# Kernel tuning notes

Hardware: AMD Instinct MI355X
Metric: run time of the kernel (lower is better)

The kernel has to match this reference:

```python
import jax, jax.numpy as jnp
import numpy as np

B, S, D, E = 2, 2048, 1024, 8
H = 2 * D          # hidden_dim = 2*n_embd
A = H // 16        # adapt_dim


def _ln(x, g, b):
    m = x.mean(-1, keepdims=True)
    v = x.var(-1, keepdims=True)
    return (x - m) * jax.lax.rsqrt(v + 1e-5) * g + b


def setup_inputs() -> dict:
    key = jax.random.key(0)
    ks = jax.random.split(key, 16)
    s = 1.0 / np.sqrt(D)        # shared-linear init scale
    sa = s * 0.01               # adapter-linear init scale
    sg = 0.01 / np.sqrt(A)      # expert adapter init scale
    f32 = jnp.float32
    return {
        "x": jax.random.normal(ks[0], (B, S, D), f32),
        "expert_weights": jax.nn.softmax(jax.random.normal(ks[1], (B * S, E), f32), -1),
        "up_w": jax.random.normal(ks[2], (H, D), f32) * s,
        "gate_w": jax.random.normal(ks[3], (H, D), f32) * s,
        "down_w": jax.random.normal(ks[4], (D, H), f32) * s,
        "pre_w": jax.random.normal(ks[5], (A, D), f32) * sa,
        "post_w": jax.random.normal(ks[6], (A, H), f32) * sa,
        "an_g": jnp.ones((A,), f32),
        "an_b": jnp.zeros((A,), f32),
        "adapt_proj_w": jax.random.normal(ks[7], (H, A), f32) * sa,
        "adapter_w": jax.random.normal(ks[8], (E, A, A), f32) * sg,
        "adapter_g": jnp.ones((E, A), f32),
        "adapter_b": jnp.zeros((E, A), f32),
        "expert_proj_w": jax.random.normal(ks[9], (H, A), f32) * sg,
        "output_proj_w": jax.random.normal(ks[10], (D, H), f32) * sg,
    }


def reference(x, expert_weights, up_w, gate_w, down_w, pre_w, post_w, an_g, an_b,
              adapt_proj_w, adapter_w, adapter_g, adapter_b, expert_proj_w, output_proj_w):
    # ---- SharedExpertMLP ----
    up = x @ up_w.T                                  # [B,S,H]
    gate = x @ gate_w.T                              # [B,S,H]
    hidden = jax.nn.silu(gate) * up                  # SwiGLU
    adapt_in = _ln(x @ pre_w.T, an_g, an_b)          # [B,S,A]
    adapt_out = _ln(hidden @ post_w.T, an_g, an_b)   # [B,S,A]
    w = jnp.einsum('bsa,bta->bst', adapt_in, adapt_out)
    w = jax.nn.silu(jnp.clip(w, -5.0, 5.0))          # clamp+SiLU score
    # explicit fp32 bmm as in original autocast-disabled block
    adapt = jnp.einsum('bst,bta->bsa',
                       w.astype(jnp.float32),
                       adapt_in.astype(jnp.float32)).astype(x.dtype)
    hidden = hidden + 0.1 * (adapt @ adapt_proj_w.T)
    shared_out = hidden @ down_w.T                   # [B,S,D] (dropout is identity in eval)

    # ---- per-token expert mixing ----
    xf = x.reshape(-1, x.shape[-1])                  # [N,D], N=B*S
    a = _ln(xf @ pre_w.T, an_g, an_b)                # [N,A]
    h = jnp.einsum('na,eca->nec', a, adapter_w)      # per-expert low-rank adapt [N,E,A]
    h = _ln(h, adapter_g[None], adapter_b[None])
    mixed = jnp.einsum('ne,nea->na', expert_weights, h)   # combine experts [N,A]
    out = (mixed @ expert_proj_w.T) @ output_proj_w.T     # [N,D]
    return shared_out + out.reshape(x.shape)
```

## Files before the change

kernel.cpp:

```cpp
#include <hip/hip_runtime.h>
#include <hip/hip_bf16.h>
#include <math.h>

#define Bq 2
#define Sq 2048
#define Dq 1024
#define Eq 8
#define Hq 2048
#define Aq 128
#define Nq (Bq*Sq)

typedef __attribute__((ext_vector_type(4))) float f32x4;
typedef __attribute__((ext_vector_type(8))) short bfrag;

__device__ __forceinline__ float silu_f(float x) {
    return x / (1.0f + expf(-x));
}
__device__ __forceinline__ unsigned short f2bf(float x) {
    unsigned u = __float_as_uint(x);
    u += 0x7fffu + ((u >> 16) & 1u);
    return (unsigned short)(u >> 16);
}
__device__ __forceinline__ float bf2f(unsigned short h) {
    return __uint_as_float(((unsigned)h) << 16);
}
__device__ __forceinline__ void gl16(const unsigned short* g, unsigned short* l) {
    __builtin_amdgcn_global_load_lds(
        (const __attribute__((address_space(1))) void*)g,
        (__attribute__((address_space(3))) void*)(void*)l, 16, 0, 0);
}

#define WAITV_BAR(N)                                            \
    asm volatile("s_waitcnt vmcnt(" #N ")" ::: "memory");       \
    __builtin_amdgcn_s_barrier();                               \
    asm volatile("" ::: "memory")
#define END_BAR()                                               \
    asm volatile("" ::: "memory");                              \
    __builtin_amdgcn_s_barrier();                               \
    asm volatile("" ::: "memory")

__global__ __launch_bounds__(256)
void convert_all(const float* __restrict__ x,  const float* __restrict__ gw,
                 const float* __restrict__ uw, const float* __restrict__ dw,
                 const float* __restrict__ pw, const float* __restrict__ ow,
                 const float* __restrict__ opw, const float* __restrict__ aw,
                 unsigned short* xh,  unsigned short* gwh, unsigned short* uwh,
                 unsigned short* dwh, unsigned short* pwh, unsigned short* powh,
                 unsigned short* oph, unsigned short* adw)
{
    const int T = 3276800;
    for (int i = blockIdx.x * 256 + threadIdx.x; i < T; i += gridDim.x * 256) {
        const float* in; unsigned short* hi; int j = i;
        if (j < 1048576)                 { in = x;   hi = xh;  }
        else if ((j -= 1048576) < 524288){ in = gw;  hi = gwh; }
        else if ((j -= 524288) < 524288) { in = uw;  hi = uwh; }
        else if ((j -= 524288) < 524288) { in = dw;  hi = dwh; }
        else if ((j -= 524288) < 32768)  { in = pw;  hi = pwh; }
        else if ((j -= 32768) < 65536)   { in = ow;  hi = powh; }
        else if ((j -= 65536) < 524288)  { in = opw; hi = oph; }
        else { j -= 524288;                in = aw;  hi = adw; }
        float4 v = ((const float4*)in)[j];
        ((ushort4*)hi)[j] = make_ushort4(f2bf(v.x), f2bf(v.y), f2bf(v.z), f2bf(v.w));
    }
}

template<typename TIN>
__global__ __launch_bounds__(256)
void transb(const TIN* __restrict__ in0, const TIN* __restrict__ in1,
            unsigned short* __restrict__ out, int R, int C)
{
    __shared__ float t[32][33];
    const TIN* in = blockIdx.z ? in1 : in0;
    if (!in1) in = in0 + (size_t)blockIdx.z * R * C;
    out += (size_t)blockIdx.z * R * C;
    int tx = threadIdx.x & 31, ty = threadIdx.x >> 5;
    int r0 = blockIdx.y * 32, c0 = blockIdx.x * 32;
#pragma unroll
    for (int j = 0; j < 4; j++) {
        TIN v = in[(size_t)(r0 + ty + j * 8) * C + c0 + tx];
        float f;
        if (sizeof(TIN) == 2) f = bf2f(*(const unsigned short*)&v);
        else                  f = *(const float*)&v;
        t[ty + j * 8][tx] = f;
    }
    __syncthreads();
#pragma unroll
    for (int j = 0; j < 4; j++)
        out[(size_t)(c0 + ty + j * 8) * R + r0 + tx] = f2bf(t[tx][ty + j * 8]);
}

template<int EPI>
__global__ __launch_bounds__(512)
void mg(const unsigned short* __restrict__ Ah, const unsigned short* __restrict__ Bh,
        void* __restrict__ Cv, int N, int K, int kchunks,
        long zA, long zB, long zC, long pz)
{
    __shared__ __align__(16) unsigned short lds[32768];

    const int tid = threadIdx.x;
    const int l   = tid & 63;
    const int w   = tid >> 6;
    const int wr  = w >> 2, wc = w & 3;
    const int bm0 = blockIdx.y * 128, bn0 = blockIdx.x * 128;
    const int bz  = blockIdx.z / kchunks;
    const int kz  = blockIdx.z - bz * kchunks;
    const int kcnt = K / kchunks;
    const int kbeg = kz * kcnt;
    const int kend = kbeg + kcnt;

    const unsigned short* A0 = Ah + (size_t)bz * zA;
    const unsigned short* B0 = Bh + (size_t)bz * zB;

    const int srow = tid >> 3;
    const int sq   = (tid & 7) ^ (srow & 7);
    const size_t aoff = (size_t)(bm0 + srow) * K + sq * 8;
    const size_t boff = (size_t)(bn0 + srow) * K + sq * 8;
    const size_t r64  = (size_t)64 * K;

    auto stage = [&](int b, int kt) {
        unsigned short* d = &lds[b * 16384 + (w << 9)];
        gl16(A0 + aoff + kt,       d + 0);
        gl16(A0 + aoff + kt + r64, d + 4096);
        gl16(B0 + boff + kt,       d + 8192);
        gl16(B0 + boff + kt + r64, d + 12288);
    };

    const int rowa = (wr * 64 + (l & 15)) * 64;
    const int rowb = (wc * 32 + (l & 15)) * 64;
    const int q0 = (((l >> 4)    ) ^ (l & 7)) << 3;
    const int q1 = (((l >> 4) + 4) ^ (l & 7)) << 3;

    f32x4 acc[4][2];
#pragma unroll
    for (int i = 0; i < 4; i++)
#pragma unroll
        for (int j = 0; j < 2; j++) acc[i][j] = (f32x4){0.f, 0.f, 0.f, 0.f};

    stage(0, kbeg);
    int cur = 0;
    for (int kt = kbeg; kt < kend; kt += 64) {
        if (kt + 64 < kend) {
            stage(cur ^ 1, kt + 64);
            WAITV_BAR(4);
        } else {
            WAITV_BAR(0);
        }
        const int cb = cur * 16384;
#pragma unroll
        for (int ks = 0; ks < 2; ks++) {
            const int qo = ks ? q1 : q0;
            bfrag a4[4], b4[2];
#pragma unroll
            for (int f = 0; f < 4; f++)
                a4[f] = *(const bfrag*)&lds[cb + rowa + f * 1024 + qo];
#pragma unroll
            for (int f = 0; f < 2; f++)
                b4[f] = *(const bfrag*)&lds[cb + 8192 + rowb + f * 1024 + qo];
#pragma unroll
            for (int i = 0; i < 4; i++)
#pragma unroll
                for (int j = 0; j < 2; j++)
                    acc[i][j] = __builtin_amdgcn_mfma_f32_16x16x32_bf16(a4[i], b4[j], acc[i][j], 0, 0, 0);
        }
        END_BAR();
        cur ^= 1;
    }

    const int crow0 = bm0 + wr * 64 + (l >> 4) * 4;
    const int ccol0 = bn0 + wc * 32 + (l & 15);
#pragma unroll
    for (int i = 0; i < 4; i++)
#pragma unroll
        for (int j = 0; j < 2; j++)
#pragma unroll
            for (int r = 0; r < 4; r++) {
                size_t idx = (size_t)(crow0 + i * 16 + r) * N + (ccol0 + j * 16);
                float v = acc[i][j][r];
                if (EPI == 0)
                    ((float*)Cv + (size_t)bz * zC + (size_t)kz * pz)[idx] = v;
                else
                    ((unsigned short*)Cv + (size_t)bz * zC)[idx] =
                        f2bf(silu_f(fminf(fmaxf(v, -5.f), 5.f)));
            }
}

__global__ __launch_bounds__(512)
void gsc(const unsigned short* __restrict__ ainh, const unsigned short* __restrict__ aouth,
         const unsigned short* __restrict__ ainT, float* __restrict__ p3)
{
    __shared__ __align__(16) unsigned short lds[65536];
    const int AIN = 0, AOUT = 16384, AINT = 32768, PB = 49152;

    const int tid = threadIdx.x;
    const int l   = tid & 63;
    const int w   = tid >> 6;
    const int wr  = w >> 2, wc = w & 3;
    const int tz  = blockIdx.x;
    const int ib  = blockIdx.y;
    const int b   = blockIdx.z;
    const long SA = (long)Sq * Aq;

    auto stage32 = [&](int base, const unsigned short* src, size_t kstride) {
#pragma unroll
        for (int rd = 0; rd < 4; rd++) {
            int grow = rd * 32 + (w << 2) + (l >> 4);
            int slot = (l & 15) ^ (grow & 15);
            gl16(src + (size_t)grow * kstride + slot * 8,
                 &lds[base + rd * 4096 + (w << 9)]);
        }
    };

    const unsigned short* ainI_src = ainh + (size_t)b * SA + (size_t)(ib * 128) * Aq;
    f32x4 acc2[4][2];
#pragma unroll
    for (int i = 0; i < 4; i++)
#pragma unroll
        for (int j = 0; j < 2; j++) acc2[i][j] = (f32x4){0.f, 0.f, 0.f, 0.f};

    {
        int tglob = tz * 2;
        stage32(AIN,  ainI_src, Aq);
        stage32(AOUT, aouth + (size_t)b * SA + (size_t)(tglob * 128) * Aq, Aq);
        stage32(AINT, ainT  + (size_t)b * SA + (size_t)(tglob * 128), Sq);
        WAITV_BAR(0);
    }

    const int rowa = (wr * 64 + (l & 15)) * 128;
    const int rowb = (wc * 32 + (l & 15)) * 128;

#pragma unroll 1
    for (int t = 0; t < 2; t++) {
        if (t == 1) {
            int tglob = tz * 2 + 1;
            stage32(AOUT, aouth + (size_t)b * SA + (size_t)(tglob * 128) * Aq, Aq);
            stage32(AINT, ainT  + (size_t)b * SA + (size_t)(tglob * 128), Sq);
            WAITV_BAR(0);
        }
        f32x4 acc1[4][2];
#pragma unroll
        for (int i = 0; i < 4; i++)
#pragma unroll
            for (int j = 0; j < 2; j++) acc1[i][j] = (f32x4){0.f, 0.f, 0.f, 0.f};
#pragma unroll
        for (int ks = 0; ks < 4; ks++) {
            const int qo = ((ks * 4 + (l >> 4)) ^ (l & 15)) << 3;
            bfrag a4[4], b4[2];
#pragma unroll
            for (int f = 0; f < 4; f++)
                a4[f] = *(const bfrag*)&lds[AIN + rowa + f * 2048 + qo];
#pragma unroll
            for (int f = 0; f < 2; f++)
                b4[f] = *(const bfrag*)&lds[AOUT + rowb + f * 2048 + qo];
#pragma unroll
            for (int i = 0; i < 4; i++)
#pragma unroll
                for (int j = 0; j < 2; j++)
                    acc1[i][j] = __builtin_amdgcn_mfma_f32_16x16x32_bf16(a4[i], b4[j], acc1[i][j], 0, 0, 0);
        }
        {
            const int prow0 = wr * 64 + (l >> 4) * 4;
            const int pcol0 = wc * 32 + (l & 15);
#pragma unroll
            for (int i = 0; i < 4; i++)
#pragma unroll
                for (int j = 0; j < 2; j++)
#pragma unroll
                    for (int r = 0; r < 4; r++) {
                        int pr = prow0 + i * 16 + r;
                        int pc = pcol0 + j * 16;
                        float v = silu_f(fminf(fmaxf(acc1[i][j][r], -5.f), 5.f));
                        lds[PB + pr * 128 + (((pc >> 3) ^ (pr & 15)) << 3) + (pc & 7)] = f2bf(v);
                    }
        }
        __syncthreads();
#pragma unroll
        for (int ks = 0; ks < 4; ks++) {
            const int qo = ((ks * 4 + (l >> 4)) ^ (l & 15)) << 3;
            bfrag a4[4], b4[2];
#pragma unroll
            for (int f = 0; f < 4; f++)
                a4[f] = *(const bfrag*)&lds[PB + rowa + f * 2048 + qo];
#pragma unroll
            for (int f = 0; f < 2; f++)
                b4[f] = *(const bfrag*)&lds[AINT + rowb + f * 2048 + qo];
#pragma unroll
            for (int i = 0; i < 4; i++)
#pragma unroll
                for (int j = 0; j < 2; j++)
                    acc2[i][j] = __builtin_amdgcn_mfma_f32_16x16x32_bf16(a4[i], b4[j], acc2[i][j], 0, 0, 0);
        }
        __syncthreads();
    }

    const int crow0 = wr * 64 + (l >> 4) * 4;
    const int ccol0 = wc * 32 + (l & 15);
    float* dst = p3 + ((size_t)(b * 8 + tz) * Sq + ib * 128) * Aq;
#pragma unroll
    for (int i = 0; i < 4; i++)
#pragma unroll
        for (int j = 0; j < 2; j++)
#pragma unroll
            for (int r = 0; r < 4; r++)
                dst[(size_t)(crow0 + i * 16 + r) * Aq + ccol0 + j * 16] = acc2[i][j][r];
}

__global__ __launch_bounds__(512)
void gup(const unsigned short* __restrict__ xh, const unsigned short* __restrict__ gwh,
         const unsigned short* __restrict__ uwh, unsigned short* __restrict__ hh)
{
    __shared__ __align__(16) unsigned short lds[24576];
    const int tid = threadIdx.x;
    const int l   = tid & 63;
    const int w   = tid >> 6;
    const int wr  = w >> 2, wc = w & 3;

    int id  = blockIdx.y * gridDim.x + blockIdx.x;
    int xcd = id & 7, j = id >> 3;
    int bx  = (xcd & 1) * 8 + (j & 7);
    int by  = (xcd >> 1) * 8 + (j >> 3);
    const int bm0 = by * 128, bn0 = bx * 128;

    const int srow = tid >> 2;
    const int sq   = (tid & 3) ^ ((srow >> 1) & 3);
    const size_t aoff = (size_t)(bm0 + srow) * Dq + sq * 8;
    const size_t boff = (size_t)(bn0 + srow) * Dq + sq * 8;

    const int rowa = (wr * 64 + (l & 15)) * 32;
    const int rowb = (wc * 32 + (l & 15)) * 32;
    const int q0 = (((l >> 4)) ^ (((l & 15) >> 1) & 3)) << 3;

    auto stage = [&](int b, int kt) {
        unsigned short* d = &lds[b * 12288 + (w << 9)];
        gl16(xh  + aoff + kt, d + 0);
        gl16(gwh + boff + kt, d + 4096);
        gl16(uwh + boff + kt, d + 8192);
    };

    f32x4 accg[4][2], accu[4][2];
#pragma unroll
    for (int i = 0; i < 4; i++)
#pragma unroll
        for (int jj = 0; jj < 2; jj++) {
            accg[i][jj] = (f32x4){0.f, 0.f, 0.f, 0.f};
            accu[i][jj] = (f32x4){0.f, 0.f, 0.f, 0.f};
        }

    stage(0, 0);
    int cur = 0;
    for (int kt = 0; kt < Dq; kt += 32) {
        if (kt + 32 < Dq) {
            stage(cur ^ 1, kt + 32);
            WAITV_BAR(3);
        } else {
            WAITV_BAR(0);
        }
        const int cb = cur * 12288;
        bfrag a4[4], g4[2], u4[2];
#pragma unroll
        for (int f = 0; f < 4; f++)
            a4[f] = *(const bfrag*)&lds[cb + rowa + f * 512 + q0];
#pragma unroll
        for (int f = 0; f < 2; f++) {
            g4[f] = *(const bfrag*)&lds[cb + 4096 + rowb + f * 512 + q0];
            u4[f] = *(const bfrag*)&lds[cb + 8192 + rowb + f * 512 + q0];
        }
#pragma unroll
        for (int i = 0; i < 4; i++)
#pragma unroll
            for (int jj = 0; jj < 2; jj++) {
                accg[i][jj] = __builtin_amdgcn_mfma_f32_16x16x32_bf16(a4[i], g4[jj], accg[i][jj], 0, 0, 0);
                accu[i][jj] = __builtin_amdgcn_mfma_f32_16x16x32_bf16(a4[i], u4[jj], accu[i][jj], 0, 0, 0);
            }
        END_BAR();
        cur ^= 1;
    }

    const int crow0 = bm0 + wr * 64 + (l >> 4) * 4;
    const int ccol0 = bn0 + wc * 32 + (l & 15);
#pragma unroll
    for (int i = 0; i < 4; i++)
#pragma unroll
        for (int jj = 0; jj < 2; jj++)
#pragma unroll
            for (int r = 0; r < 4; r++) {
                size_t idx = (size_t)(crow0 + i * 16 + r) * Hq + (ccol0 + jj * 16);
                hh[idx] = f2bf(silu_f(accg[i][jj][r]) * accu[i][jj][r]);
            }
}

__global__ __launch_bounds__(512)
void gfinal(const unsigned short* __restrict__ hh, const unsigned short* __restrict__ dwh,
            const unsigned short* __restrict__ acat, const unsigned short* __restrict__ kcat,
            float* __restrict__ out)
{
    __shared__ __align__(16) unsigned short lds[49152];
    const int tid = threadIdx.x;
    const int l   = tid & 63;
    const int w   = tid >> 6;
    const int wr  = w >> 2, wc = w & 3;

    int nb  = gridDim.x * gridDim.y;
    int id  = blockIdx.y * gridDim.x + blockIdx.x;
    int id2 = (id & 7) * (nb >> 3) + (id >> 3);
    int bx  = id2 % gridDim.x, by = id2 / gridDim.x;
    const int bm0 = by * 128, bn0 = bx * 128;

    const int srow = tid >> 3;
    const int sq   = (tid & 7) ^ (srow & 7);
    const int rowa = (wr * 64 + (l & 15)) * 64;
    const int rowb = (wc * 32 + (l & 15)) * 64;
    const int q0 = (((l >> 4)    ) ^ (l & 7)) << 3;
    const int q1 = (((l >> 4) + 4) ^ (l & 7)) << 3;

    f32x4 acc[4][2];
#pragma unroll
    for (int i = 0; i < 4; i++)
#pragma unroll
        for (int j = 0; j < 2; j++) acc[i][j] = (f32x4){0.f, 0.f, 0.f, 0.f};

    {
        const size_t aoff = (size_t)(bm0 + srow) * Hq + sq * 8;
        const size_t boff = (size_t)(bn0 + srow) * Hq + sq * 8;
        const size_t r64  = (size_t)64 * Hq;
        auto stage = [&](int b, int kt) {
            unsigned short* d = &lds[b * 16384 + (w << 9)];
            gl16(hh  + aoff + kt,       d + 0);
            gl16(hh  + aoff + kt + r64, d + 4096);
            gl16(dwh + boff + kt,       d + 8192);
            gl16(dwh + boff + kt + r64, d + 12288);
        };
        stage(0, 0);
        stage(1, 64);
        int cur = 0;
        for (int kt = 0; kt < Hq; kt += 64) {
            if (kt + 64 < Hq) { WAITV_BAR(4); } else { WAITV_BAR(0); }
            if (kt + 128 < Hq) {
                int nb3 = (cur + 2 >= 3) ? cur - 1 : cur + 2;
                stage(nb3, kt + 128);
            }
            const int cb = cur * 16384;
#pragma unroll
            for (int ks = 0; ks < 2; ks++) {
                const int qo = ks ? q1 : q0;
                bfrag a4[4], b4[2];
#pragma unroll
                for (int f = 0; f < 4; f++)
                    a4[f] = *(const bfrag*)&lds[cb + rowa + f * 1024 + qo];
#pragma unroll
                for (int f = 0; f < 2; f++)
                    b4[f] = *(const bfrag*)&lds[cb + 8192 + rowb + f * 1024 + qo];
#pragma unroll
                for (int i = 0; i < 4; i++)
#pragma unroll
                    for (int j = 0; j < 2; j++)
                        acc[i][j] = __builtin_amdgcn_mfma_f32_16x16x32_bf16(a4[i], b4[j], acc[i][j], 0, 0, 0);
            }
            cur = (cur == 2) ? 0 : cur + 1;
        }
    }
    END_BAR();
    {
        const size_t aoff = (size_t)(bm0 + srow) * 256 + sq * 8;
        const size_t boff = (size_t)(bn0 + srow) * 256 + sq * 8;
        const size_t r64  = (size_t)64 * 256;
        auto stage2 = [&](int b, int kt) {
            unsigned short* d = &lds[b * 16384 + (w << 9)];
            gl16(acat + aoff + kt,       d + 0);
            gl16(acat + aoff + kt + r64, d + 4096);
            gl16(kcat + boff + kt,       d + 8192);
            gl16(kcat + boff + kt + r64, d + 12288);
        };
        stage2(0, 0);
        stage2(1, 64);
        int cur = 0;
        for (int kt = 0; kt < 256; kt += 64) {
            if (kt + 64 < 256) { WAITV_BAR(4); } else { WAITV_BAR(0); }
            if (kt + 128 < 256) {
                int nb3 = (cur + 2 >= 3) ? cur - 1 : cur + 2;
                stage2(nb3, kt + 128);
            }
            const int cb = cur * 16384;
#pragma unroll
            for (int ks = 0; ks < 2; ks++) {
                const int qo = ks ? q1 : q0;
                bfrag a4[4], b4[2];
#pragma unroll
                for (int f = 0; f < 4; f++)
                    a4[f] = *(const bfrag*)&lds[cb + rowa + f * 1024 + qo];
#pragma unroll
                for (int f = 0; f < 2; f++)
                    b4[f] = *(const bfrag*)&lds[cb + 8192 + rowb + f * 1024 + qo];
#pragma unroll
                for (int i = 0; i < 4; i++)
#pragma unroll
                    for (int j = 0; j < 2; j++)
                        acc[i][j] = __builtin_amdgcn_mfma_f32_16x16x32_bf16(a4[i], b4[j], acc[i][j], 0, 0, 0);
            }
            cur = (cur == 2) ? 0 : cur + 1;
        }
    }

    const int crow0 = bm0 + wr * 64 + (l >> 4) * 4;
    const int ccol0 = bn0 + wc * 32 + (l & 15);
#pragma unroll
    for (int i = 0; i < 4; i++)
#pragma unroll
        for (int j = 0; j < 2; j++)
#pragma unroll
            for (int r = 0; r < 4; r++)
                out[(size_t)(crow0 + i * 16 + r) * Dq + ccol0 + j * 16] = acc[i][j][r];
}

template<int NZ>
__global__ __launch_bounds__(256)
void rln(const float* __restrict__ p, unsigned short* __restrict__ oh,
         const float* __restrict__ g, const float* __restrict__ b, long pstride)
{
    int row  = blockIdx.x * 4 + (threadIdx.x >> 6);
    int lane = threadIdx.x & 63;
    long base = (long)row * Aq;
    float x0 = 0.f, x1 = 0.f;
#pragma unroll
    for (int z = 0; z < NZ; z++) {
        x0 += p[base + z * pstride + lane];
        x1 += p[base + z * pstride + lane + 64];
    }
    float s  = x0 + x1;
    float ss = x0 * x0 + x1 * x1;
#pragma unroll
    for (int off = 32; off > 0; off >>= 1) {
        s  += __shfl_xor(s, off);
        ss += __shfl_xor(ss, off);
    }
    float m  = s * (1.0f / Aq);
    float v  = ss * (1.0f / Aq) - m * m;
    float rs = rsqrtf(v + 1e-5f);
    oh[base + lane]      = f2bf((x0 - m) * rs * g[lane]      + b[lane]);
    oh[base + lane + 64] = f2bf((x1 - m) * rs * g[lane + 64] + b[lane + 64]);
}

template<int NZ>
__global__ __launch_bounds__(256)
void rbf(const float* __restrict__ p, unsigned short* __restrict__ o,
         int rowsPerB, float scale, int total, int ostride, int ocol, int ocolStep)
{
    int i = blockIdx.x * 256 + threadIdx.x;
    if (i >= total) return;
    int n = i >> 7, a = i & 127;
    int bz = n / rowsPerB, s = n - bz * rowsPerB;
    long base = ((long)bz * NZ) * rowsPerB * Aq + (long)s * Aq + a;
    float acc = 0.f;
#pragma unroll
    for (int z = 0; z < NZ; z++) acc += p[base + (long)z * rowsPerB * Aq];
    o[(long)s * ostride + (ocol + bz * ocolStep) + a +
      (ocolStep ? 0 : (long)bz * rowsPerB * ostride)] = f2bf(acc * scale);
}

__global__ __launch_bounds__(256)
void mix_ln(const float* __restrict__ h, const float* __restrict__ ew,
            const float* __restrict__ g, const float* __restrict__ bb,
            unsigned short* __restrict__ acat)
{
    int n    = blockIdx.x * 4 + (threadIdx.x >> 6);
    int lane = threadIdx.x & 63;
    float a0 = 0.0f, a1 = 0.0f;
#pragma unroll
    for (int e = 0; e < Eq; e++) {
        const float* r = h + ((long)e * Nq + n) * Aq;
        float x0 = r[lane], x1 = r[lane + 64];
        float s  = x0 + x1;
        float ss = x0 * x0 + x1 * x1;
#pragma unroll
        for (int off = 32; off > 0; off >>= 1) {
            s  += __shfl_xor(s, off);
            ss += __shfl_xor(ss, off);
        }
        float m  = s * (1.0f / Aq);
        float v  = ss * (1.0f / Aq) - m * m;
        float rs = rsqrtf(v + 1e-5f);
        float wv = ew[(long)n * Eq + e];
        a0 += wv * ((x0 - m) * rs * g[e * Aq + lane]      + bb[e * Aq + lane]);
        a1 += wv * ((x1 - m) * rs * g[e * Aq + lane + 64] + bb[e * Aq + lane + 64]);
    }
    acat[(long)n * 256 + 128 + lane]      = f2bf(a0);
    acat[(long)n * 256 + 128 + lane + 64] = f2bf(a1);
}

extern "C" void kernel_launch(void* const* d_in, const int* in_sizes, int n_in,
                              void* d_out, int out_size, void* d_ws, size_t ws_size,
                              hipStream_t stream)
{
    const float* x             = (const float*)d_in[0];
    const float* ew            = (const float*)d_in[1];
    const float* up_w          = (const float*)d_in[2];
    const float* gate_w        = (const float*)d_in[3];
    const float* down_w        = (const float*)d_in[4];
    const float* pre_w         = (const float*)d_in[5];
    const float* post_w        = (const float*)d_in[6];
    const float* an_g          = (const float*)d_in[7];
    const float* an_b          = (const float*)d_in[8];
    const float* adapt_proj_w  = (const float*)d_in[9];
    const float* adapter_w     = (const float*)d_in[10];
    const float* adapter_g     = (const float*)d_in[11];
    const float* adapter_b     = (const float*)d_in[12];
    const float* expert_proj_w = (const float*)d_in[13];
    const float* output_proj_w = (const float*)d_in[14];
    float* out = (float*)d_out;

#define OFF(kb) ((char*)d_ws + (size_t)(kb) * 1024)
    float* kdp  = (float*)OFF(0);
    float* wfp  = (float*)OFF(8192);
    float* p1   = (float*)OFF(16384);
    float* p2   = (float*)OFF(0);
    float* p3   = (float*)OFF(0);
    float* h_e  = (float*)OFF(0);
    unsigned short* hh   = (unsigned short*)OFF(32768);
    unsigned short* xh   = (unsigned short*)OFF(49152);
    unsigned short* gwh  = (unsigned short*)OFF(57344);
    unsigned short* uwh  = (unsigned short*)OFF(61440);
    unsigned short* dwh  = (unsigned short*)OFF(65536);
    unsigned short* oph  = (unsigned short*)OFF(69632);
    unsigned short* pwh  = (unsigned short*)OFF(73728);
    unsigned short* powh = (unsigned short*)OFF(73984);
    unsigned short* apT  = (unsigned short*)OFF(74496);
    unsigned short* epT  = (unsigned short*)OFF(75008);
    unsigned short* ainh = (unsigned short*)OFF(75520);
    unsigned short* ainT = (unsigned short*)OFF(76544);
    unsigned short* aouth= (unsigned short*)OFF(77568);
    unsigned short* adw  = (unsigned short*)OFF(78592);
    unsigned short* kcat = (unsigned short*)OFF(78848);
    unsigned short* acat = (unsigned short*)OFF(79360);
#undef OFF

    dim3 blk(256), blk512(512);
    const long NA = (long)Nq * Aq;
    const long SA = (long)Sq * Aq;
    const long SS = (long)Sq * Sq;

    convert_all<<<dim3(2048), blk, 0, stream>>>(x, gate_w, up_w, down_w, pre_w, post_w,
        output_proj_w, adapter_w, xh, gwh, uwh, dwh, pwh, powh, oph, adw);
    transb<float><<<dim3(4, 64, 2), blk, 0, stream>>>(adapt_proj_w, expert_proj_w,
        apT, Hq, Aq);

    mg<0><<<dim3(1, 8, 32), blk512, 0, stream>>>(dwh, apT, kdp, Aq, Hq, 16,
        (long)Dq * Hq, (long)Aq * Hq, (long)16 * Dq * Aq, (long)Dq * Aq);
    rbf<16><<<dim3(1024), blk, 0, stream>>>(kdp, kcat, Dq, 1.0f, 2 * Dq * Aq, 256, 0, 128);

    mg<0><<<dim3(1, 32, 8), blk512, 0, stream>>>(xh, pwh, p1, Aq, Dq, 8, 0, 0, 0, NA);
    rln<8><<<dim3(1024), blk, 0, stream>>>(p1, ainh, an_g, an_b, NA);
    transb<unsigned short><<<dim3(4, 64, 2), blk, 0, stream>>>(ainh, nullptr,
        ainT, Sq, Aq);

    gup<<<dim3(16, 32), blk512, 0, stream>>>(xh, gwh, uwh, hh);

    mg<0><<<dim3(1, 32, 8), blk512, 0, stream>>>(hh, powh, p2, Aq, Hq, 8, 0, 0, 0, NA);
    rln<8><<<dim3(1024), blk, 0, stream>>>(p2, aouth, an_g, an_b, NA);

    gsc<<<dim3(8, 16, 2), blk512, 0, stream>>>(ainh, aouth, ainT, p3);
    rbf<8><<<dim3(2048), blk, 0, stream>>>(p3, acat, Sq, 0.1f, Nq * Aq, 256, 0, 0);

    mg<0><<<dim3(1, 32, 8), blk512, 0, stream>>>(ainh, adw, h_e, Aq, Aq, 1,
        0, (long)Aq * Aq, NA, 0);
    mix_ln<<<dim3(1024), blk, 0, stream>>>(h_e, ew, adapter_g, adapter_b, acat);

    gfinal<<<dim3(8, 32), blk512, 0, stream>>>(hh, dwh, acat, kcat, out);
}
```

Baseline: 164.6 us.

## Fold transposes and reductions into neighboring kernels to cut launches

Merges the weight transpose into the conversion kernel as extra blocks. The adapt_in transpose now happens inside the layernorm kernel through a strided write. The expert-adapter GEMM moves earlier and writes bf16 instead of fp32. The p3 split-K reduction and the expert mixing layernorm are merged into one tail kernel. This removes three launches and halves the h_e traffic, at the cost of uncoalesced transposed stores and bf16 rounding of the expert activations before layernorm.

```diff
diff --git a/kernel.cpp b/kernel.cpp
--- a/kernel.cpp
+++ b/kernel.cpp
@@ -44,12 +44,32 @@
                  const float* __restrict__ uw, const float* __restrict__ dw,
                  const float* __restrict__ pw, const float* __restrict__ ow,
                  const float* __restrict__ opw, const float* __restrict__ aw,
+                 const float* __restrict__ apw, const float* __restrict__ epw,
                  unsigned short* xh,  unsigned short* gwh, unsigned short* uwh,
                  unsigned short* dwh, unsigned short* pwh, unsigned short* powh,
-                 unsigned short* oph, unsigned short* adw)
-{
+                 unsigned short* oph, unsigned short* adw, unsigned short* apT)
+{
+    __shared__ float t[32][33];
+    if (blockIdx.x >= 2048) {
+        int bid = blockIdx.x - 2048;
+        int z   = bid >> 8;
+        int rem = bid & 255;
+        int bx  = rem & 3, by = rem >> 2;
+        const float* in = z ? epw : apw;
+        unsigned short* out = apT + (size_t)z * Hq * Aq;
+        int tx = threadIdx.x & 31, ty = threadIdx.x >> 5;
+        int r0 = by * 32, c0 = bx * 32;
+#pragma unroll
+        for (int j = 0; j < 4; j++)
+            t[ty + j * 8][tx] = in[(size_t)(r0 + ty + j * 8) * Aq + c0 + tx];
+        __syncthreads();
+#pragma unroll
+        for (int j = 0; j < 4; j++)
+            out[(size_t)(c0 + ty + j * 8) * Hq + r0 + tx] = f2bf(t[tx][ty + j * 8]);
+        return;
+    }
     const int T = 3276800;
-    for (int i = blockIdx.x * 256 + threadIdx.x; i < T; i += gridDim.x * 256) {
+    for (int i = blockIdx.x * 256 + threadIdx.x; i < T; i += 2048 * 256) {
         const float* in; unsigned short* hi; int j = i;
         if (j < 1048576)                 { in = x;   hi = xh;  }
         else if ((j -= 1048576) < 524288){ in = gw;  hi = gwh; }
@@ -64,31 +84,6 @@
     }
 }
 
-template<typename TIN>
-__global__ __launch_bounds__(256)
-void transb(const TIN* __restrict__ in0, const TIN* __restrict__ in1,
-            unsigned short* __restrict__ out, int R, int C)
-{
-    __shared__ float t[32][33];
-    const TIN* in = blockIdx.z ? in1 : in0;
-    if (!in1) in = in0 + (size_t)blockIdx.z * R * C;
-    out += (size_t)blockIdx.z * R * C;
-    int tx = threadIdx.x & 31, ty = threadIdx.x >> 5;
-    int r0 = blockIdx.y * 32, c0 = blockIdx.x * 32;
-#pragma unroll
-    for (int j = 0; j < 4; j++) {
-        TIN v = in[(size_t)(r0 + ty + j * 8) * C + c0 + tx];
-        float f;
-        if (sizeof(TIN) == 2) f = bf2f(*(const unsigned short*)&v);
-        else                  f = *(const float*)&v;
-        t[ty + j * 8][tx] = f;
-    }
-    __syncthreads();
-#pragma unroll
-    for (int j = 0; j < 4; j++)
-        out[(size_t)(c0 + ty + j * 8) * R + r0 + tx] = f2bf(t[tx][ty + j * 8]);
-}
-
 template<int EPI>
 __global__ __launch_bounds__(512)
 void mg(const unsigned short* __restrict__ Ah, const unsigned short* __restrict__ Bh,
@@ -178,9 +173,11 @@
                 float v = acc[i][j][r];
                 if (EPI == 0)
                     ((float*)Cv + (size_t)bz * zC + (size_t)kz * pz)[idx] = v;
-                else
+                else if (EPI == 1)
                     ((unsigned short*)Cv + (size_t)bz * zC)[idx] =
                         f2bf(silu_f(fminf(fmaxf(v, -5.f), 5.f)));
+                else
+                    ((unsigned short*)Cv + (size_t)bz * zC)[idx] = f2bf(v);
             }
 }
 
@@ -511,9 +508,10 @@
                 out[(size_t)(crow0 + i * 16 + r) * Dq + ccol0 + j * 16] = acc[i][j][r];
 }
 
-template<int NZ>
+template<int NZ, bool WT>
 __global__ __launch_bounds__(256)
 void rln(const float* __restrict__ p, unsigned short* __restrict__ oh,
+         unsigned short* __restrict__ aT,
          const float* __restrict__ g, const float* __restrict__ b, long pstride)
 {
     int row  = blockIdx.x * 4 + (threadIdx.x >> 6);
@@ -535,8 +533,16 @@
     float m  = s * (1.0f / Aq);
     float v  = ss * (1.0f / Aq) - m * m;
     float rs = rsqrtf(v + 1e-5f);
-    oh[base + lane]      = f2bf((x0 - m) * rs * g[lane]      + b[lane]);
-    oh[base + lane + 64] = f2bf((x1 - m) * rs * g[lane + 64] + b[lane + 64]);
+    unsigned short h0 = f2bf((x0 - m) * rs * g[lane]      + b[lane]);
+    unsigned short h1 = f2bf((x1 - m) * rs * g[lane + 64] + b[lane + 64]);
+    oh[base + lane]      = h0;
+    oh[base + lane + 64] = h1;
+    if (WT) {
+        int bb2 = row >> 11, sidx = row & 2047;
+        unsigned short* t = aT + (size_t)bb2 * Sq * Aq + sidx;
+        t[(size_t)lane * Sq]        = h0;
+        t[(size_t)(lane + 64) * Sq] = h1;
+    }
 }
 
 template<int NZ>
@@ -557,17 +563,28 @@
 }
 
 __global__ __launch_bounds__(256)
-void mix_ln(const float* __restrict__ h, const float* __restrict__ ew,
-            const float* __restrict__ g, const float* __restrict__ bb,
-            unsigned short* __restrict__ acat)
-{
-    int n    = blockIdx.x * 4 + (threadIdx.x >> 6);
+void tailk(const float* __restrict__ p3, const unsigned short* __restrict__ he,
+           const float* __restrict__ ew, const float* __restrict__ g,
+           const float* __restrict__ bb, unsigned short* __restrict__ acat)
+{
+    if (blockIdx.x < 2048) {
+        int i = blockIdx.x * 256 + threadIdx.x;
+        int n = i >> 7, a = i & 127;
+        int bz = n >> 11, s = n & 2047;
+        long base = ((long)bz * 8) * Sq * Aq + (long)s * Aq + a;
+        float acc = 0.f;
+#pragma unroll
+        for (int z = 0; z < 8; z++) acc += p3[base + (long)z * Sq * Aq];
+        acat[(long)n * 256 + a] = f2bf(acc * 0.1f);
+        return;
+    }
+    int n    = (blockIdx.x - 2048) * 4 + (threadIdx.x >> 6);
     int lane = threadIdx.x & 63;
     float a0 = 0.0f, a1 = 0.0f;
 #pragma unroll
     for (int e = 0; e < Eq; e++) {
-        const float* r = h + ((long)e * Nq + n) * Aq;
-        float x0 = r[lane], x1 = r[lane + 64];
+        const unsigned short* r = he + ((long)e * Nq + n) * Aq;
+        float x0 = bf2f(r[lane]), x1 = bf2f(r[lane + 64]);
         float s  = x0 + x1;
         float ss = x0 * x0 + x1 * x1;
 #pragma unroll
@@ -609,11 +626,10 @@
 
 #define OFF(kb) ((char*)d_ws + (size_t)(kb) * 1024)
     float* kdp  = (float*)OFF(0);
-    float* wfp  = (float*)OFF(8192);
     float* p1   = (float*)OFF(16384);
     float* p2   = (float*)OFF(0);
     float* p3   = (float*)OFF(0);
-    float* h_e  = (float*)OFF(0);
+    unsigned short* he = (unsigned short*)OFF(16384);
     unsigned short* hh   = (unsigned short*)OFF(32768);
     unsigned short* xh   = (unsigned short*)OFF(49152);
     unsigned short* gwh  = (unsigned short*)OFF(57344);
@@ -631,37 +647,33 @@
     unsigned short* kcat = (unsigned short*)OFF(78848);
     unsigned short* acat = (unsigned short*)OFF(79360);
 #undef OFF
+    (void)epT;
 
     dim3 blk(256), blk512(512);
     const long NA = (long)Nq * Aq;
-    const long SA = (long)Sq * Aq;
-    const long SS = (long)Sq * Sq;
-
-    convert_all<<<dim3(2048), blk, 0, stream>>>(x, gate_w, up_w, down_w, pre_w, post_w,
-        output_proj_w, adapter_w, xh, gwh, uwh, dwh, pwh, powh, oph, adw);
-    transb<float><<<dim3(4, 64, 2), blk, 0, stream>>>(adapt_proj_w, expert_proj_w,
-        apT, Hq, Aq);
+
+    convert_all<<<dim3(2560), blk, 0, stream>>>(x, gate_w, up_w, down_w, pre_w,
+        post_w, output_proj_w, adapter_w, adapt_proj_w, expert_proj_w,
+        xh, gwh, uwh, dwh, pwh, powh, oph, adw, apT);
 
     mg<0><<<dim3(1, 8, 32), blk512, 0, stream>>>(dwh, apT, kdp, Aq, Hq, 16,
         (long)Dq * Hq, (long)Aq * Hq, (long)16 * Dq * Aq, (long)Dq * Aq);
     rbf<16><<<dim3(1024), blk, 0, stream>>>(kdp, kcat, Dq, 1.0f, 2 * Dq * Aq, 256, 0, 128);
 
     mg<0><<<dim3(1, 32, 8), blk512, 0, stream>>>(xh, pwh, p1, Aq, Dq, 8, 0, 0, 0, NA);
-    rln<8><<<dim3(1024), blk, 0, stream>>>(p1, ainh, an_g, an_b, NA);
-    transb<unsigned short><<<dim3(4, 64, 2), blk, 0, stream>>>(ainh, nullptr,
-        ainT, Sq, Aq);
+    rln<8, true><<<dim3(1024), blk, 0, stream>>>(p1, ainh, ainT, an_g, an_b, NA);
+
+    mg<2><<<dim3(1, 32, 8), blk512, 0, stream>>>(ainh, adw, he, Aq, Aq, 1,
+        0, (long)Aq * Aq, NA, 0);
 
     gup<<<dim3(16, 32), blk512, 0, stream>>>(xh, gwh, uwh, hh);
 
     mg<0><<<dim3(1, 32, 8), blk512, 0, stream>>>(hh, powh, p2, Aq, Hq, 8, 0, 0, 0, NA);
-    rln<8><<<dim3(1024), blk, 0, stream>>>(p2, aouth, an_g, an_b, NA);
+    rln<8, false><<<dim3(1024), blk, 0, stream>>>(p2, aouth, nullptr, an_g, an_b, NA);
 
     gsc<<<dim3(8, 16, 2), blk512, 0, stream>>>(ainh, aouth, ainT, p3);
-    rbf<8><<<dim3(2048), blk, 0, stream>>>(p3, acat, Sq, 0.1f, Nq * Aq, 256, 0, 0);
-
-    mg<0><<<dim3(1, 32, 8), blk512, 0, stream>>>(ainh, adw, h_e, Aq, Aq, 1,
-        0, (long)Aq * Aq, NA, 0);
-    mix_ln<<<dim3(1024), blk, 0, stream>>>(h_e, ew, adapter_g, adapter_b, acat);
+
+    tailk<<<dim3(3072), blk, 0, stream>>>(p3, he, ew, adapter_g, adapter_b, acat);
 
     gfinal<<<dim3(8, 32), blk512, 0, stream>>>(hh, dwh, acat, kcat, out);
 }
```

Measured after the change: 163.0 us. Within noise of the previous version (-1.0%).
